# Kernel tuning notes

Measured on AMD Instinct MI355X. Metric: run time of the kernel, lower is better.

Reference implementation:

```python
import jax, jax.numpy as jnp
import numpy as np

L, H, D, HS = 6, 8, 512, 64
EPS = 1e-5


def _ln(x, g, b):
    m = jnp.mean(x, -1, keepdims=True)
    v = jnp.mean((x - m) ** 2, -1, keepdims=True)
    return (x - m) * jax.lax.rsqrt(v + EPS) * g + b


def _posenc(T, C):
    pos = jnp.arange(T, dtype=jnp.float32)[:, None]
    div = jnp.exp(jnp.arange(0, C, 2, dtype=jnp.float32) * (-jnp.log(10000.0) / C))
    pe = jnp.zeros((T, C), jnp.float32)
    pe = pe.at[:, 0::2].set(jnp.sin(pos * div))
    pe = pe.at[:, 1::2].set(jnp.cos(pos * div))
    return pe


def setup_inputs() -> dict:
    B, T, F, V, E, O = 8, 1024, 32, 7, 16, 49
    key = jax.random.key(0)
    ks = jax.random.split(key, 16)
    s = 0.02
    inp = {
        'code': jax.random.randint(ks[0], (B, T, F), 0, V),
        'lengths': jax.random.randint(ks[1], (B,), T // 2, T + 1),
        'emb': s * jax.random.normal(ks[2], (V, E), jnp.float32),
        'Wq': s * jax.random.normal(ks[3], (L, H, D, HS), jnp.float32),
        'Wk': s * jax.random.normal(ks[4], (L, H, D, HS), jnp.float32),
        'Wv': s * jax.random.normal(ks[5], (L, H, D, HS), jnp.float32),
        'Wo': s * jax.random.normal(ks[6], (L, D, D), jnp.float32),
        'bo': jnp.zeros((L, D), jnp.float32),
        'W1': s * jax.random.normal(ks[7], (L, D, 4 * D), jnp.float32),
        'b1': jnp.zeros((L, 4 * D), jnp.float32),
        'W2': s * jax.random.normal(ks[8], (L, 4 * D, D), jnp.float32),
        'b2': jnp.zeros((L, D), jnp.float32),
        'ln1_g': jnp.ones((L, D), jnp.float32),
        'ln1_b': jnp.zeros((L, D), jnp.float32),
        'ln2_g': jnp.ones((L, D), jnp.float32),
        'ln2_b': jnp.zeros((L, D), jnp.float32),
        'lnf_g': jnp.ones((D,), jnp.float32),
        'lnf_b': jnp.zeros((D,), jnp.float32),
        'attn_w': s * jax.random.normal(ks[9], (D, 1), jnp.float32),
        'attn_b': jnp.zeros((1,), jnp.float32),
        'head_w': s * jax.random.normal(ks[10], (D, 49), jnp.float32),
        'head_b': jnp.zeros((49,), jnp.float32),
    }
    return inp


def reference(code, lengths, emb, Wq, Wk, Wv, Wo, bo, W1, b1, W2, b2,
              ln1_g, ln1_b, ln2_g, ln2_b, lnf_g, lnf_b,
              attn_w, attn_b, head_w, head_b):
    B, T, F = code.shape
    # token embedding (B,T,F,E) -> (B,T,D) plus sinusoidal positions
    x = emb[code].reshape(B, T, D) + _posenc(T, D)
    mask = jnp.arange(T) < lengths[:, None]          # (B,T) valid positions
    col_mask = mask[:, None, None, :]                # mask key columns
    row_mask = mask[:, None, :, None]                # zero padded query rows
    for l in range(L):
        xn = _ln(x, ln1_g[l], ln1_b[l])
        q = jnp.einsum('btd,hde->bhte', xn, Wq[l])
        k = jnp.einsum('btd,hde->bhte', xn, Wk[l])
        v = jnp.einsum('btd,hde->bhte', xn, Wv[l])
        wei = jnp.einsum('bhte,bhse->bhts', q, k) * (HS ** -0.5)
        wei = jnp.where(col_mask, wei, -jnp.inf)
        wei = jax.nn.softmax(wei, axis=-1)
        wei = jnp.where(row_mask, wei, 0.0)
        o = jnp.einsum('bhts,bhse->bthe', wei, v).reshape(B, T, H * HS)
        x = x + o @ Wo[l] + bo[l]
        xn = _ln(x, ln2_g[l], ln2_b[l])
        x = x + jax.nn.gelu(xn @ W1[l] + b1[l], approximate=False) @ W2[l] + b2[l]
    x = _ln(x, lnf_g, lnf_b)
    # attention pooling over time
    scores = x @ attn_w + attn_b                     # (B,T,1)
    scores = jnp.where(mask[:, :, None], scores, -jnp.inf)
    aw = jax.nn.softmax(scores, axis=1)
    summary = jnp.sum(aw * x, axis=1)                # (B,D)
    logits = summary @ head_w + head_b               # (B,49)
    return logits
```

## Files before the change

kernel.cpp:

```cpp
#include <hip/hip_runtime.h>
#include <math.h>

#define TT 1024
#define BB 8
#define DD 512
#define HH 8
#define HSZ 64
#define LL 6
#define FF4 2048

typedef __attribute__((ext_vector_type(8))) short short8;
typedef __attribute__((ext_vector_type(4))) float floatx4;
typedef unsigned short ushort_t;
typedef unsigned int uint_t;

__device__ __forceinline__ ushort_t f2bf(float f) {
  uint_t u = __float_as_uint(f);
  u += 0x7fff + ((u >> 16) & 1);
  return (ushort_t)(u >> 16);
}
__device__ __forceinline__ float bf2f(ushort_t h) {
  return __uint_as_float(((uint_t)h) << 16);
}

typedef const __attribute__((address_space(1))) uint_t* gas_t;
typedef __attribute__((address_space(3))) uint_t* las_t;
__device__ __forceinline__ void stage16(const ushort_t* g, ushort_t* l) {
  __builtin_amdgcn_global_load_lds((gas_t)g, (las_t)l, 16, 0, 0);
}


__global__ __launch_bounds__(256) void k_embed(const int* __restrict__ code,
                                               const float* __restrict__ emb,
                                               float* __restrict__ x,
                                               const int* __restrict__ lengths) {
  int idx = blockIdx.x * 256 + threadIdx.x;
  int c = idx & (DD - 1);
  int bt = idx >> 9;
  int t = bt & (TT - 1);
  if (t >= lengths[bt >> 10]) return;
  int f = c >> 4, e = c & 15;
  int vv = code[bt * 32 + f];
  int i = c >> 1;
  float freq = expf((float)(2 * i) * (-9.210340371976184f / 512.f));
  float ang = (float)t * freq;
  float pe = (c & 1) ? cosf(ang) : sinf(ang);
  x[idx] = emb[vv * 16 + e] + pe;
}

__global__ __launch_bounds__(256) void k_ln(const float* __restrict__ x,
                                            ushort_t* __restrict__ yB,
                                            float* __restrict__ yF,
                                            const float* __restrict__ g,
                                            const float* __restrict__ b,
                                            const float* __restrict__ aw,
                                            const float* __restrict__ ab,
                                            float* __restrict__ scores,
                                            const int* __restrict__ lengths) {
  int row0 = blockIdx.x * 4;
  if ((row0 & (TT - 1)) >= lengths[row0 >> 10]) return;
  int wave = threadIdx.x >> 6, lane = threadIdx.x & 63;
  int row = row0 + wave;
  const float* xr = x + (size_t)row * DD;
  float v[8];
  *(float4*)&v[0] = *(const float4*)(xr + lane * 8);
  *(float4*)&v[4] = *(const float4*)(xr + lane * 8 + 4);
  float s = 0.f;
#pragma unroll
  for (int j = 0; j < 8; ++j) s += v[j];
#pragma unroll
  for (int off = 32; off; off >>= 1) s += __shfl_down(s, off, 64);
  float mean = __shfl(s, 0, 64) * (1.f / DD);
  float qv = 0.f;
#pragma unroll
  for (int j = 0; j < 8; ++j) { float d = v[j] - mean; qv += d * d; }
#pragma unroll
  for (int off = 32; off; off >>= 1) qv += __shfl_down(qv, off, 64);
  float rs = rsqrtf(__shfl(qv, 0, 64) * (1.f / DD) + 1e-5f);
  float ov[8];
  float sdot = 0.f;
#pragma unroll
  for (int e = 0; e < 8; ++e) {
    int c = lane * 8 + e;
    ov[e] = (v[e] - mean) * rs * g[c] + b[c];
    if (scores) sdot += ov[e] * aw[c];
  }
  if (yB) {
    short8 o8;
#pragma unroll
    for (int e = 0; e < 8; ++e) o8[e] = (short)f2bf(ov[e]);
    size_t ad = (((size_t)(row >> 4) * 16 + (lane >> 2)) << 9) + ((lane & 3) * 16 + (row & 15)) * 8;
    *(short8*)(yB + ad) = o8;
  } else {
    float* yr = yF + (size_t)row * DD + lane * 8;
    *(float4*)yr = *(float4*)&ov[0];
    *(float4*)(yr + 4) = *(float4*)&ov[4];
  }
  if (scores) {
#pragma unroll
    for (int off = 32; off; off >>= 1) sdot += __shfl_down(sdot, off, 64);
    if (lane == 0) scores[row] = sdot + ab[0];
  }
}

__global__ __launch_bounds__(256) void k_packw(const float* __restrict__ in,
                                               ushort_t* __restrict__ out,
                                               int Nin, long in_ms, int nh,
                                               long os_l, int nblk, int Kout) {
  __shared__ float t4[64][65];
  int mz = blockIdx.z;
  const float* ip = in + (size_t)mz * in_ms;
  ushort_t* op = out + (size_t)(mz / nh) * os_l;
  int nbase = (mz % nh) * nblk + blockIdx.y * 64;
  int k0 = blockIdx.x * 64;
  int cc = threadIdx.x & 63, r0 = threadIdx.x >> 6;
#pragma unroll
  for (int i = 0; i < 16; ++i) {
    int r = r0 * 16 + i;
    t4[r][cc] = ip[(size_t)(k0 + r) * Nin + (nbase - (mz % nh) * nblk) + cc];
  }
  __syncthreads();
#pragma unroll
  for (int half = 0; half < 2; ++half) {
    int c = threadIdx.x + half * 256;
    int joct = c >> 6, nl = c & 63;
    int n = nbase + nl, k = k0 + joct * 8;
    short8 v8;
#pragma unroll
    for (int e = 0; e < 8; ++e) v8[e] = (short)f2bf(t4[joct * 8 + e][nl]);
    size_t ad = (((size_t)(n >> 4) * (Kout >> 5) + (k >> 5)) << 9) + (((k >> 3) & 3) * 16 + (n & 15)) * 8;
    *(short8*)(op + ad) = v8;
  }
}

template <int BM, int BN>
__global__ __launch_bounds__(256, (BM == 128) ? 3 : 4) void k_agemm(const ushort_t* __restrict__ Apk,
                                                                    const ushort_t* __restrict__ Bpk,
                                                                    const float* __restrict__ resid,
                                                                    const float* __restrict__ bias,
                                                                    float* __restrict__ outF,
                                                                    ushort_t* __restrict__ outB,
                                                                    int M, int N, int K, int mode,
                                                                    const int* __restrict__ lengths) {
  constexpr int MT = BM / 32;
  constexpr int NT = BN / 32;
  constexpr int NA = BM / 16;
  constexpr int NB = BN / 16;
  constexpr int NFRAG = NA + NB;
  constexpr int NF = NFRAG / 4;
  constexpr int BUFU = NFRAG * 512;
  __shared__ ushort_t lds[(BM == 128) ? 20480 : 2 * NFRAG * 512];

  const int tid = threadIdx.x;
  const int w = tid >> 6, lane = tid & 63;
  const int quad = lane >> 4, l16 = lane & 15;
  const int gx = N / BN;
  int id = blockIdx.x;
  int bx = (id >> 3) % gx;
  int by = (id / (8 * gx)) * 8 + (id & 7);
  const int row0 = by * BM, col0 = bx * BN;
  if (lengths && (row0 & (TT - 1)) >= lengths[row0 >> 10]) return;
  const int nk = K >> 5;

  const int wrow0 = row0 + (w >> 1) * (BM / 2);
  const int wcol0 = col0 + (w & 1) * (BN / 2);
  const int ar16 = (w >> 1) * MT;
  const int bc16 = NA + (w & 1) * NT;

  const ushort_t* gsrc[NF];
  int slot[NF];
#pragma unroll
  for (int i = 0; i < NF; ++i) {
    int f = w * NF + i;
    if (f < NA)
      gsrc[i] = Apk + (((size_t)((row0 >> 4) + f) * nk) << 9) + lane * 8;
    else
      gsrc[i] = Bpk + (((size_t)((col0 >> 4) + (f - NA)) * nk) << 9) + lane * 8;
    slot[i] = f * 512;
  }

  floatx4 acc[MT][NT] = {};

#pragma unroll
  for (int i = 0; i < NF; ++i) stage16(gsrc[i], &lds[slot[i]]);
  __syncthreads();

  int bufo = 0;
  for (int kc = 0; kc + 1 < nk; ++kc) {
    const int nbufo = bufo ^ BUFU;
#pragma unroll
    for (int i = 0; i < NF; ++i)
      stage16(gsrc[i] + ((size_t)(kc + 1) << 9), &lds[nbufo + slot[i]]);
    short8 af[MT], bfv[NT];
#pragma unroll
    for (int mt = 0; mt < MT; ++mt) af[mt] = *(const short8*)&lds[bufo + (ar16 + mt) * 512 + lane * 8];
#pragma unroll
    for (int nt = 0; nt < NT; ++nt) bfv[nt] = *(const short8*)&lds[bufo + (bc16 + nt) * 512 + lane * 8];
#pragma unroll
    for (int mt = 0; mt < MT; ++mt)
#pragma unroll
      for (int nt = 0; nt < NT; ++nt)
        acc[mt][nt] = __builtin_amdgcn_mfma_f32_16x16x32_bf16(af[mt], bfv[nt], acc[mt][nt], 0, 0, 0);
    __syncthreads();
    bufo = nbufo;
  }
  {
    short8 af[MT], bfv[NT];
#pragma unroll
    for (int mt = 0; mt < MT; ++mt) af[mt] = *(const short8*)&lds[bufo + (ar16 + mt) * 512 + lane * 8];
#pragma unroll
    for (int nt = 0; nt < NT; ++nt) bfv[nt] = *(const short8*)&lds[bufo + (bc16 + nt) * 512 + lane * 8];
#pragma unroll
    for (int mt = 0; mt < MT; ++mt)
#pragma unroll
      for (int nt = 0; nt < NT; ++nt)
        acc[mt][nt] = __builtin_amdgcn_mfma_f32_16x16x32_bf16(af[mt], bfv[nt], acc[mt][nt], 0, 0, 0);
  }

  if (BM == 128 && mode == 2) {
    __syncthreads();
    ushort_t* Cb = &lds[w * 5120];
#pragma unroll
    for (int mt = 0; mt < MT; ++mt)
#pragma unroll
      for (int nt = 0; nt < NT; ++nt) {
        floatx4 a4 = acc[mt][nt];
#pragma unroll
        for (int r = 0; r < 4; ++r) {
          float val = a4[r] + bias[wcol0 + nt * 16 + l16];
          val = 0.5f * val * (1.f + erff(val * 0.7071067811865475f));
          Cb[(mt * 16 + quad * 4 + r) * 80 + nt * 16 + l16] = f2bf(val);
        }
      }
#pragma unroll
    for (int mt2 = 0; mt2 < 4; ++mt2)
#pragma unroll
      for (int kt2 = 0; kt2 < 2; ++kt2) {
        short8 v8 = *(const short8*)&Cb[(mt2 * 16 + l16) * 80 + kt2 * 32 + quad * 8];
        size_t ad = ((((size_t)(wrow0 >> 4) + mt2) * (N >> 5) + (wcol0 >> 5) + kt2) << 9) + lane * 8;
        *(short8*)(outB + ad) = v8;
      }
  } else {
    const float qscale = (mode == 3 && col0 < 512) ? 0.125f : 1.0f;
#pragma unroll
    for (int mt = 0; mt < MT; ++mt)
#pragma unroll
      for (int nt = 0; nt < NT; ++nt) {
        floatx4 a4 = acc[mt][nt];
#pragma unroll
        for (int r = 0; r < 4; ++r) {
          int row = wrow0 + mt * 16 + quad * 4 + r;
          int col = wcol0 + nt * 16 + l16;
          float val = a4[r];
          if (bias) val += bias[col];
          size_t idx = (size_t)row * N + col;
          if (mode == 1) outF[idx] = val + resid[idx];
          else outB[idx] = f2bf(val * qscale);
        }
      }
  }
}

__global__ __launch_bounds__(256) void k_attn(const ushort_t* __restrict__ qkv,
                                              const int* __restrict__ lengths,
                                              ushort_t* __restrict__ o) {
  __shared__ ushort_t Ks[64 * 72];
  __shared__ ushort_t Vt[64 * 72];
  __shared__ ushort_t Ps[4][16 * 72];
  const int tid = threadIdx.x;
  const int w = tid >> 6, lane = tid & 63;
  const int quad = lane >> 4, l16 = lane & 15;
  const int tile = blockIdx.x & 15;
  const int bh = blockIdx.x >> 4;
  const int b = bh >> 3, h = bh & 7;
  const int len = lengths[b];
  if (tile * 64 >= len) return;
  const int tqa = tile * 64 + w * 16 + l16;
  const ushort_t* qp = qkv + ((size_t)(b * TT + tqa)) * 1536 + h * HSZ + quad * 8;
  short8 qf0 = *(const short8*)qp;
  short8 qf1 = *(const short8*)(qp + 32);
  floatx4 oacc[4] = {};
  float lsum[4] = {0.f, 0.f, 0.f, 0.f};
  const int skey = tid >> 2, sseg = (tid & 3) << 4;
  const int vkp = (tid & 31) << 1, vds = (tid >> 5) << 3;
  const int nkt = (len + 63) >> 6;
  for (int kt = 0; kt < nkt; ++kt) {
    const int s0 = kt * 64;
    __syncthreads();
    {
      const ushort_t* kp = qkv + ((size_t)(b * TT + s0 + skey)) * 1536 + 512 + h * HSZ + sseg;
      short8 k0 = *(const short8*)kp;
      short8 k1 = *(const short8*)(kp + 8);
      *(short8*)&Ks[skey * 72 + sseg] = k0;
      *(short8*)&Ks[skey * 72 + sseg + 8] = k1;
      const ushort_t* vp0 = qkv + ((size_t)(b * TT + s0 + vkp)) * 1536 + 1024 + h * HSZ + vds;
      short8 v0 = *(const short8*)vp0;
      short8 v1 = *(const short8*)(vp0 + 1536);
#pragma unroll
      for (int i = 0; i < 8; ++i) {
        ushort2 pr;
        pr.x = (ushort_t)v0[i];
        pr.y = (ushort_t)v1[i];
        *(ushort2*)&Vt[(vds + i) * 72 + vkp] = pr;
      }
    }
    __syncthreads();
    floatx4 sacc[4] = {};
#pragma unroll
    for (int nt = 0; nt < 4; ++nt) {
      short8 kf0 = *(const short8*)&Ks[(nt * 16 + l16) * 72 + quad * 8];
      short8 kf1 = *(const short8*)&Ks[(nt * 16 + l16) * 72 + 32 + quad * 8];
      sacc[nt] = __builtin_amdgcn_mfma_f32_16x16x32_bf16(qf0, kf0, sacc[nt], 0, 0, 0);
      sacc[nt] = __builtin_amdgcn_mfma_f32_16x16x32_bf16(qf1, kf1, sacc[nt], 0, 0, 0);
    }
    float p[4][4];
    if (kt == nkt - 1) {
#pragma unroll
      for (int nt = 0; nt < 4; ++nt) {
        bool valid = (s0 + nt * 16 + l16 < len);
#pragma unroll
        for (int r = 0; r < 4; ++r) p[nt][r] = valid ? __expf(sacc[nt][r]) : 0.f;
      }
    } else {
#pragma unroll
      for (int nt = 0; nt < 4; ++nt)
#pragma unroll
        for (int r = 0; r < 4; ++r) p[nt][r] = __expf(sacc[nt][r]);
    }
#pragma unroll
    for (int r = 0; r < 4; ++r)
#pragma unroll
      for (int nt = 0; nt < 4; ++nt) {
        lsum[r] += p[nt][r];
        Ps[w][(quad * 4 + r) * 72 + nt * 16 + l16] = f2bf(p[nt][r]);
      }
    short8 pf0 = *(const short8*)&Ps[w][l16 * 72 + quad * 8];
    short8 pf1 = *(const short8*)&Ps[w][l16 * 72 + 32 + quad * 8];
#pragma unroll
    for (int nt = 0; nt < 4; ++nt) {
      short8 vf0 = *(const short8*)&Vt[(nt * 16 + l16) * 72 + quad * 8];
      short8 vf1 = *(const short8*)&Vt[(nt * 16 + l16) * 72 + 32 + quad * 8];
      oacc[nt] = __builtin_amdgcn_mfma_f32_16x16x32_bf16(pf0, vf0, oacc[nt], 0, 0, 0);
      oacc[nt] = __builtin_amdgcn_mfma_f32_16x16x32_bf16(pf1, vf1, oacc[nt], 0, 0, 0);
    }
  }
#pragma unroll
  for (int off = 1; off < 16; off <<= 1) {
#pragma unroll
    for (int r = 0; r < 4; ++r) lsum[r] += __shfl_xor(lsum[r], off, 64);
  }
#pragma unroll
  for (int r = 0; r < 4; ++r) {
    int t = tile * 64 + w * 16 + quad * 4 + r;
    float inv = (t < len) ? 1.f / lsum[r] : 0.f;
#pragma unroll
    for (int nt = 0; nt < 4; ++nt)
      Ps[w][(quad * 4 + r) * 72 + nt * 16 + l16] = f2bf(oacc[nt][r] * inv);
  }
  const int mtile = b * 64 + tile * 4 + w;
#pragma unroll
  for (int kt2 = 0; kt2 < 2; ++kt2) {
    short8 v8 = *(const short8*)&Ps[w][l16 * 72 + kt2 * 32 + quad * 8];
    size_t ad = (((size_t)mtile * 16 + h * 2 + kt2) << 9) + lane * 8;
    *(short8*)(o + ad) = v8;
  }
}

__global__ __launch_bounds__(256) void k_softw(const float* __restrict__ scores,
                                               const int* __restrict__ lengths,
                                               float* __restrict__ wts) {
  __shared__ float red[8];
  int tid = threadIdx.x, b = blockIdx.x;
  int len = lengths[b];
  const float* sb = scores + b * TT;
  float m = -1e30f;
  for (int t = tid; t < len; t += 256) m = fmaxf(m, sb[t]);
#pragma unroll
  for (int off = 32; off; off >>= 1) m = fmaxf(m, __shfl_down(m, off, 64));
  if ((tid & 63) == 0) red[tid >> 6] = m;
  __syncthreads();
  m = fmaxf(fmaxf(red[0], red[1]), fmaxf(red[2], red[3]));
  float ssum = 0.f;
  for (int t = tid; t < len; t += 256) ssum += __expf(sb[t] - m);
#pragma unroll
  for (int off = 32; off; off >>= 1) ssum += __shfl_down(ssum, off, 64);
  if ((tid & 63) == 0) red[4 + (tid >> 6)] = ssum;
  __syncthreads();
  float inv = 1.f / (red[4] + red[5] + red[6] + red[7]);
  for (int t = tid; t < TT; t += 256)
    wts[b * TT + t] = (t < len) ? __expf(sb[t] - m) * inv : 0.f;
}

__global__ __launch_bounds__(256) void k_wsum(const float* __restrict__ xf,
                                              const float* __restrict__ wts,
                                              float* __restrict__ partial,
                                              const int* __restrict__ lengths) {
  int b = blockIdx.x, c = blockIdx.y, tid = threadIdx.x;
  float* pp = partial + ((size_t)b * 16 + c) * DD;
  if (c * 64 >= lengths[b]) {
    pp[tid] = 0.f;
    pp[tid + 256] = 0.f;
    return;
  }
  const float* xb = xf + ((size_t)b * TT + c * 64) * DD;
  const float* wb = wts + b * TT + c * 64;
  float a0 = 0.f, a1 = 0.f;
  for (int t = 0; t < 64; ++t) {
    float wv = wb[t];
    a0 += wv * xb[(size_t)t * DD + tid];
    a1 += wv * xb[(size_t)t * DD + tid + 256];
  }
  pp[tid] = a0;
  pp[tid + 256] = a1;
}

__global__ __launch_bounds__(64) void k_head(const float* __restrict__ partial,
                                             const float* __restrict__ head_w,
                                             const float* __restrict__ head_b,
                                             float* __restrict__ out) {
  __shared__ float ssum[DD];
  int b = blockIdx.x, tid = threadIdx.x;
  for (int d = tid; d < DD; d += 64) {
    float s = 0.f;
#pragma unroll
    for (int c = 0; c < 16; ++c) s += partial[((size_t)b * 16 + c) * DD + d];
    ssum[d] = s;
  }
  __syncthreads();
  if (tid < 49) {
    float s = head_b[tid];
    for (int d = 0; d < DD; ++d) s += ssum[d] * head_w[d * 49 + tid];
    out[b * 49 + tid] = s;
  }
}

extern "C" void kernel_launch(void* const* d_in, const int* in_sizes, int n_in,
                              void* d_out, int out_size, void* d_ws, size_t ws_size,
                              hipStream_t stream) {
  const int* code = (const int*)d_in[0];
  const int* lengths = (const int*)d_in[1];
  const float* emb = (const float*)d_in[2];
  const float* Wq = (const float*)d_in[3];
  const float* Wk = (const float*)d_in[4];
  const float* Wv = (const float*)d_in[5];
  const float* Wo = (const float*)d_in[6];
  const float* bo = (const float*)d_in[7];
  const float* W1 = (const float*)d_in[8];
  const float* b1 = (const float*)d_in[9];
  const float* W2 = (const float*)d_in[10];
  const float* b2 = (const float*)d_in[11];
  const float* ln1_g = (const float*)d_in[12];
  const float* ln1_b = (const float*)d_in[13];
  const float* ln2_g = (const float*)d_in[14];
  const float* ln2_b = (const float*)d_in[15];
  const float* lnf_g = (const float*)d_in[16];
  const float* lnf_b = (const float*)d_in[17];
  const float* attn_w = (const float*)d_in[18];
  const float* attn_b = (const float*)d_in[19];
  const float* head_w = (const float*)d_in[20];
  const float* head_b = (const float*)d_in[21];
  float* out = (float*)d_out;

  const size_t NTOK = (size_t)BB * TT;
  float* x = (float*)d_ws;
  ushort_t* xn = (ushort_t*)(x + NTOK * DD);
  ushort_t* un = xn + NTOK * DD;
  ushort_t* qkv = un;
  ushort_t* h1 = un;
  float* xf = (float*)un;
  ushort_t* wqpk = un + (size_t)NTOK * FF4;
  ushort_t* wopk = wqpk + (size_t)LL * 1536 * 512;
  ushort_t* w1pk = wopk + (size_t)LL * 512 * 512;
  ushort_t* w2pk = w1pk + (size_t)LL * 512 * FF4;
  float* scores = (float*)(w2pk + (size_t)LL * FF4 * 512);
  float* wts = scores + NTOK;
  float* partial = wts + NTOK;

  k_packw<<<dim3(8, 1, 48), 256, 0, stream>>>(Wq, wqpk,              64, (long)512 * 64, 8, (long)1536 * 512, 64, 512);
  k_packw<<<dim3(8, 1, 48), 256, 0, stream>>>(Wk, wqpk + 512 * 512,  64, (long)512 * 64, 8, (long)1536 * 512, 64, 512);
  k_packw<<<dim3(8, 1, 48), 256, 0, stream>>>(Wv, wqpk + 1024 * 512, 64, (long)512 * 64, 8, (long)1536 * 512, 64, 512);
  k_packw<<<dim3(8, 8, 6), 256, 0, stream>>>(Wo, wopk, 512, (long)512 * 512, 1, (long)512 * 512, 0, 512);
  k_packw<<<dim3(8, 32, 6), 256, 0, stream>>>(W1, w1pk, 2048, (long)512 * 2048, 1, (long)2048 * 512, 0, 512);
  k_packw<<<dim3(32, 8, 6), 256, 0, stream>>>(W2, w2pk, 512, (long)2048 * 512, 1, (long)512 * 2048, 0, 2048);

  k_embed<<<dim3((unsigned)((NTOK * DD) / 256)), dim3(256), 0, stream>>>(code, emb, x, lengths);

  for (int l = 0; l < LL; ++l) {
    k_ln<<<dim3(NTOK / 4), 256, 0, stream>>>(x, xn, nullptr, ln1_g + l * DD, ln1_b + l * DD,
                                             nullptr, nullptr, nullptr, lengths);
    k_agemm<128, 128><<<dim3(768), 256, 0, stream>>>(xn, wqpk + (size_t)l * 1536 * 512, nullptr, nullptr,
                                                     nullptr, qkv, (int)NTOK, 1536, 512, 3, lengths);
    k_attn<<<dim3(BB * HH * (TT / 64)), 256, 0, stream>>>(qkv, lengths, xn);
    k_agemm<64, 64><<<dim3(1024), 256, 0, stream>>>(xn, wopk + (size_t)l * 512 * 512, x, bo + l * DD,
                                                    x, nullptr, (int)NTOK, 512, 512, 1, lengths);
    k_ln<<<dim3(NTOK / 4), 256, 0, stream>>>(x, xn, nullptr, ln2_g + l * DD, ln2_b + l * DD,
                                             nullptr, nullptr, nullptr, lengths);
    k_agemm<128, 128><<<dim3(1024), 256, 0, stream>>>(xn, w1pk + (size_t)l * 512 * FF4, nullptr, b1 + l * FF4,
                                                      nullptr, h1, (int)NTOK, FF4, 512, 2, lengths);
    k_agemm<64, 64><<<dim3(1024), 256, 0, stream>>>(h1, w2pk + (size_t)l * FF4 * 512, x, b2 + l * DD,
                                                    x, nullptr, (int)NTOK, 512, 2048, 1, lengths);
  }
  k_ln<<<dim3(NTOK / 4), 256, 0, stream>>>(x, nullptr, xf, lnf_g, lnf_b,
                                           attn_w, attn_b, scores, lengths);
  k_softw<<<dim3(BB), 256, 0, stream>>>(scores, lengths, wts);
  k_wsum<<<dim3(BB, 16), 256, 0, stream>>>(xf, wts, partial, lengths);
  k_head<<<dim3(BB), 64, 0, stream>>>(partial, head_w, head_b, out);
}
```

Baseline: 1.236 ms.

## Deepen GEMM global-to-LDS prefetch pipeline with explicit vmcnt waits

Restructures the k_agemm main loop so smaller tiles use a 4-stage LDS ring buffer (128-row tiles keep 2 stages). Explicit s_waitcnt vmcnt counts plus raw barriers replace __syncthreads, so several k-chunks of async global_load_lds stay in flight while MFMA runs on an earlier chunk. This is meant to hide global memory latency better. It costs more LDS for the smaller tiles, which may reduce occupancy, and correctness depends on the hardcoded vmcnt values matching the number of loads issued per stage.

```diff
diff --git a/kernel.cpp b/kernel.cpp
--- a/kernel.cpp
+++ b/kernel.cpp
@@ -28,6 +28,9 @@
 __device__ __forceinline__ void stage16(const ushort_t* g, ushort_t* l) {
   __builtin_amdgcn_global_load_lds((gas_t)g, (las_t)l, 16, 0, 0);
 }
+
+#define VMWAIT(n) asm volatile("s_waitcnt vmcnt(" #n ")" ::: "memory")
+#define MEMFENCE() asm volatile("" ::: "memory")
 
 
 __global__ __launch_bounds__(256) void k_embed(const int* __restrict__ code,
@@ -149,7 +152,8 @@
   constexpr int NFRAG = NA + NB;
   constexpr int NF = NFRAG / 4;
   constexpr int BUFU = NFRAG * 512;
-  __shared__ ushort_t lds[(BM == 128) ? 20480 : 2 * NFRAG * 512];
+  constexpr int NBUF = (BM == 128) ? 2 : 4;
+  __shared__ ushort_t lds[(BM == 128) ? 20480 : NBUF * BUFU];
 
   const int tid = threadIdx.x;
   const int w = tid >> 6, lane = tid & 63;
@@ -181,40 +185,58 @@
 
   floatx4 acc[MT][NT] = {};
 
-#pragma unroll
-  for (int i = 0; i < NF; ++i) stage16(gsrc[i], &lds[slot[i]]);
-  __syncthreads();
-
-  int bufo = 0;
-  for (int kc = 0; kc + 1 < nk; ++kc) {
-    const int nbufo = bufo ^ BUFU;
-#pragma unroll
-    for (int i = 0; i < NF; ++i)
-      stage16(gsrc[i] + ((size_t)(kc + 1) << 9), &lds[nbufo + slot[i]]);
+  auto computeStep = [&](int bb) {
+    const int base = bb * BUFU;
     short8 af[MT], bfv[NT];
 #pragma unroll
-    for (int mt = 0; mt < MT; ++mt) af[mt] = *(const short8*)&lds[bufo + (ar16 + mt) * 512 + lane * 8];
-#pragma unroll
-    for (int nt = 0; nt < NT; ++nt) bfv[nt] = *(const short8*)&lds[bufo + (bc16 + nt) * 512 + lane * 8];
+    for (int mt = 0; mt < MT; ++mt) af[mt] = *(const short8*)&lds[base + (ar16 + mt) * 512 + lane * 8];
+#pragma unroll
+    for (int nt = 0; nt < NT; ++nt) bfv[nt] = *(const short8*)&lds[base + (bc16 + nt) * 512 + lane * 8];
 #pragma unroll
     for (int mt = 0; mt < MT; ++mt)
 #pragma unroll
       for (int nt = 0; nt < NT; ++nt)
         acc[mt][nt] = __builtin_amdgcn_mfma_f32_16x16x32_bf16(af[mt], bfv[nt], acc[mt][nt], 0, 0, 0);
-    __syncthreads();
-    bufo = nbufo;
-  }
-  {
-    short8 af[MT], bfv[NT];
-#pragma unroll
-    for (int mt = 0; mt < MT; ++mt) af[mt] = *(const short8*)&lds[bufo + (ar16 + mt) * 512 + lane * 8];
-#pragma unroll
-    for (int nt = 0; nt < NT; ++nt) bfv[nt] = *(const short8*)&lds[bufo + (bc16 + nt) * 512 + lane * 8];
-#pragma unroll
-    for (int mt = 0; mt < MT; ++mt)
-#pragma unroll
-      for (int nt = 0; nt < NT; ++nt)
-        acc[mt][nt] = __builtin_amdgcn_mfma_f32_16x16x32_bf16(af[mt], bfv[nt], acc[mt][nt], 0, 0, 0);
+  };
+
+#pragma unroll
+  for (int p = 0; p < NBUF - 1; ++p)
+#pragma unroll
+    for (int i = 0; i < NF; ++i)
+      stage16(gsrc[i] + ((size_t)p << 9), &lds[p * BUFU + slot[i]]);
+
+  int kc = 0;
+  for (; kc + NBUF - 1 < nk; ++kc) {
+    const int sslot = (kc + NBUF - 1) & (NBUF - 1);
+#pragma unroll
+    for (int i = 0; i < NF; ++i)
+      stage16(gsrc[i] + ((size_t)(kc + NBUF - 1) << 9), &lds[sslot * BUFU + slot[i]]);
+    if constexpr (BM == 128) VMWAIT(4);
+    else VMWAIT(6);
+    __builtin_amdgcn_s_barrier();
+    MEMFENCE();
+    computeStep(kc & (NBUF - 1));
+    MEMFENCE();
+    __builtin_amdgcn_s_barrier();
+  }
+  if constexpr (NBUF == 2) {
+    VMWAIT(0);
+    __builtin_amdgcn_s_barrier();
+    MEMFENCE();
+    computeStep(kc & 1);
+  } else {
+    VMWAIT(4);
+    __builtin_amdgcn_s_barrier();
+    MEMFENCE();
+    computeStep(kc & 3);
+    VMWAIT(2);
+    __builtin_amdgcn_s_barrier();
+    MEMFENCE();
+    computeStep((kc + 1) & 3);
+    VMWAIT(0);
+    __builtin_amdgcn_s_barrier();
+    MEMFENCE();
+    computeStep((kc + 2) & 3);
   }
 
   if (BM == 128 && mode == 2) {
```

After: 1.211 ms. 1.02x faster.
